# Kernel tuning notes

Measured on AMD Instinct MI355X. Metric: run time of the kernel, lower is better.

Reference implementation:

```python
import jax, jax.numpy as jnp
import numpy as np
from jax import lax

D, N, M_HIST, H, H_STU, T = 256, 128, 512, 32, 20, 256
ETA = 1e-3


def _hankel(m):
    # standard spectral-filtering Hankel: Z[i,j] = 2 / ((i+j)^3 - (i+j)), 1-indexed
    idx = np.arange(1, m + 1, dtype=np.float64)
    s = idx[:, None] + idx[None, :]
    return 2.0 / (s ** 3 - s)


def setup_inputs() -> dict:
    key = jax.random.key(0)
    ks = jax.random.split(key, 10)
    ev, evec = np.linalg.eigh(_hankel(M_HIST))
    phi = jnp.asarray(evec[:, -H:], jnp.float32)          # (m, h)
    sigma = jnp.asarray(ev[-H:], jnp.float32)             # (h,) positive
    phi_stu = jnp.asarray(evec[:, -H_STU:], jnp.float32)  # (m, 20)
    A = 0.05 * jax.random.normal(ks[0], (D, D), jnp.float32)
    B = 0.05 * jax.random.normal(ks[1], (D, N), jnp.float32)
    q = jax.random.normal(ks[2], (D, D), jnp.float32)
    Q = 0.1 * (q @ q.T) / D                                # PSD state cost
    r = jax.random.normal(ks[3], (N, N), jnp.float32)
    R = 0.1 * (r @ r.T) / N                                # PSD control cost
    K = 0.01 * jax.random.normal(ks[4], (N, D), jnp.float32)  # stand-in LQR gain
    M0 = 0.005 * jax.random.normal(ks[5], (H, N, D), jnp.float32)
    M_stu = 0.003 * jax.random.normal(ks[6], (H_STU, D, N), jnp.float32)
    x0 = 0.1 * jax.random.normal(ks[7], (D, 1), jnp.float32)
    W0 = jnp.zeros((D, M_HIST), jnp.float32).at[:, 0].set(
        0.1 * jax.random.normal(ks[8], (D,), jnp.float32))
    U0 = jnp.zeros((N, M_HIST), jnp.float32)
    return {"A": A, "B": B, "Q": Q, "R": R, "K": K, "phi": phi,
            "sigma": sigma, "phi_stu": phi_stu, "M0": M0, "M_stu": M_stu,
            "x0": x0, "W0": W0, "U0": U0}


def reference(A, B, Q, R, K, phi, sigma, phi_stu, M0, M_stu, x0, W0, U0):
    sig4 = sigma ** 0.25  # (h,)

    def step(carry, _):
        x, W, U, M = carry  # x:(d,1) W:(d,m) U:(n,m) M:(h,n,d)

        def cost_fn(M_):
            v = W @ phi                                        # (d, h)
            cn = jnp.einsum('h,hnd,dh->n', sig4, M_, v)[:, None]  # (n,1)
            u = -K @ x + cn                                    # flag=False branch
            cost = (x.T @ Q @ x + u.T @ R @ u)[0, 0]
            return cost, u

        (cost, u), gM = jax.value_and_grad(cost_fn, has_aux=True)(M)
        # u_t_history.roll + write detached u
        U2 = jnp.roll(U, 1, axis=1).at[:, 0].set(lax.stop_gradient(u)[:, 0])
        # x_next = sum_i M_stu[i] @ (U2 @ phi_stu[:, i])
        x_next = jnp.einsum('kdn,nk->d', M_stu, U2 @ phi_stu)[:, None]
        new_w = x_next - A @ x - B @ u
        W2 = jnp.roll(W, 1, axis=1).at[:, 0].set(lax.stop_gradient(new_w)[:, 0])
        M2 = M - ETA * gM  # inline SGD on M only (matches manual update)
        return (lax.stop_gradient(x_next), W2, U2, M2), cost

    _, losses = lax.scan(step, (x0, W0, U0, M0), None, length=T)
    return losses  # (T,)
```

## Files before the change

kernel.cpp:

```cpp
#include <hip/hip_runtime.h>

#define Dd 256
#define Nn 128
#define Hh 32
#define HSk 20
#define Tt 256
#define NWG 128
#define NT 256
#define ETAf 1e-3f

__device__ __forceinline__ unsigned ld_ag(const unsigned* p) {
  return __hip_atomic_load(p, __ATOMIC_RELAXED, __HIP_MEMORY_SCOPE_AGENT);
}
__device__ __forceinline__ void st_ag(unsigned* p, unsigned v) {
  __hip_atomic_store(p, v, __ATOMIC_RELAXED, __HIP_MEMORY_SCOPE_AGENT);
}
__device__ __forceinline__ float ldg_c(const float* p) {
  return __hip_atomic_load(p, __ATOMIC_RELAXED, __HIP_MEMORY_SCOPE_AGENT);
}
__device__ __forceinline__ void stg_c(float* p, float v) {
  __hip_atomic_store(p, v, __ATOMIC_RELAXED, __HIP_MEMORY_SCOPE_AGENT);
}

__device__ __forceinline__ void grid_sync(unsigned* flags, unsigned* gen, unsigned b) {
  asm volatile("s_waitcnt vmcnt(0)" ::: "memory");
  __syncthreads();
  if (blockIdx.x == 0) {
    const int t = threadIdx.x;
    if (t > 0 && t < NWG) {
      while (ld_ag(&flags[t * 16]) < b) __builtin_amdgcn_s_sleep(1);
    }
    __syncthreads();
    if (t == 0) st_ag(gen, b);
  } else if (threadIdx.x == 0) {
    st_ag(&flags[blockIdx.x * 16], b);
    while (ld_ag(gen) < b) __builtin_amdgcn_s_sleep(1);
  }
  asm volatile("" ::: "memory");
  __syncthreads();
}

__global__ void init_bar_kernel(unsigned* bar, int n) {
  for (int i = threadIdx.x; i < n; i += blockDim.x) bar[i] = 0u;
}

__global__ __launch_bounds__(NT, 1)
void osf_main(const float* __restrict__ Am, const float* __restrict__ Bm,
              const float* __restrict__ Qmat, const float* __restrict__ Rm,
              const float* __restrict__ Km, const float* __restrict__ phi,
              const float* __restrict__ sigma, const float* __restrict__ phis,
              const float* __restrict__ M0, const float* __restrict__ Ms,
              const float* __restrict__ x0, const float* __restrict__ W0,
              float* __restrict__ out, unsigned* __restrict__ bar,
              float* __restrict__ fws) {
  const int g = blockIdx.x;
  const int tid = threadIdx.x;

  unsigned* flags = bar;
  unsigned* gen = bar + NWG * 16;

  float* cnp  = fws;
  float* vbuf = cnp + Hh * Nn;
  float* phT  = vbuf + Hh * Dd;
  float* kx   = phT + HSk * Nn;
  float* xs   = kx + Nn;
  float* u2   = xs + Tt * Dd;

  __shared__ float s_u[Nn], s_part[2][Nn], s_urow[Tt], s_w[2][Tt];
  __shared__ float s_x[Dd], s_S[2][Nn], s_A[2][Dd], s_B[2][Nn], s_K[Dd];
  __shared__ float s_g[32], s_xh[2], s_red[NT], s_red4[NT], s_w0[2];

  const int h = g >> 2;
  const int n0 = (g & 3) * 32;
  const int jj = tid >> 3;
  const int dsub = tid & 7;
  const float sig4h = sqrtf(sqrtf(sigma[h]));

  for (int i = tid; i < Dd; i += NT) {
    s_A[0][i] = Am[(2 * g) * Dd + i];
    s_A[1][i] = Am[(2 * g + 1) * Dd + i];
    s_K[i] = Km[g * Dd + i];
  }
  for (int i = tid; i < Nn; i += NT) {
    float a0 = 0.f, a1 = 0.f;
    for (int k = 0; k < HSk; ++k) {
      a0 += phis[k] * Ms[(k * Dd + 2 * g) * Nn + i];
      a1 += phis[k] * Ms[(k * Dd + 2 * g + 1) * Nn + i];
    }
    s_S[0][i] = a0;
    s_S[1][i] = a1;
    s_B[0][i] = Bm[(2 * g) * Nn + i];
    s_B[1][i] = Bm[(2 * g + 1) * Nn + i];
  }
  if (tid < 2) s_w0[tid] = W0[(2 * g + tid) * 512];

  float Mreg[32], vp[32];
  {
    const float* mp = M0 + ((size_t)(h * Nn + n0 + jj) * Dd + dsub * 32);
#pragma unroll
    for (int e = 0; e < 32; ++e) {
      Mreg[e] = mp[e];
      vp[e] = 0.f;
    }
  }
  __syncthreads();

  unsigned b = 0;
  for (int t = 0;; ++t) {
    if (t > 0) {
      {
        const int n = tid & 127, hh = tid >> 7;
        float p = 0.f;
        const float* cp = cnp + (hh * 16) * Nn + n;
#pragma unroll
        for (int q = 0; q < 16; ++q) p += ldg_c(cp + q * Nn);
        s_part[hh][n] = p;
      }
      __syncthreads();
      if (tid < Nn) s_u[tid] = s_part[0][tid] + s_part[1][tid] - ldg_c(&kx[tid]);
      __syncthreads();
      if (tid < Nn && ((t - 1) & 127) == g) u2[(size_t)(t - 1) * Nn + tid] = s_u[tid];
      if (tid == 0) s_urow[t - 1] = s_u[g];
      {
        float p = 0.f;
        const float* rr = Rm + (n0 + jj) * Nn + dsub * 16;
#pragma unroll
        for (int q = 0; q < 16; ++q) p += rr[q] * s_u[dsub * 16 + q];
        p += __shfl_xor(p, 1);
        p += __shfl_xor(p, 2);
        p += __shfl_xor(p, 4);
        if (dsub == 0) s_g[jj] = 2.f * p;
      }
      if (t < Tt && tid < 128) {
        const int dd = tid >> 6, l = tid & 63;
        float pS = s_S[dd][l] * s_u[l] + s_S[dd][l + 64] * s_u[l + 64];
        float pB = s_B[dd][l] * s_u[l] + s_B[dd][l + 64] * s_u[l + 64];
        float pA = 0.f;
#pragma unroll
        for (int q = 0; q < 4; ++q) pA += s_A[dd][l + 64 * q] * s_x[l + 64 * q];
#pragma unroll
        for (int off = 1; off < 64; off <<= 1) {
          pS += __shfl_xor(pS, off);
          pB += __shfl_xor(pB, off);
          pA += __shfl_xor(pA, off);
        }
        if (l == 0) {
          const float xt = s_xh[dd] + pS;
          s_w[dd][t - 1] = xt - pA - pB;
          stg_c(&xs[(size_t)t * Dd + 2 * g + dd], xt);
        }
      }
      __syncthreads();
    }
    if (t == Tt) break;

    {
      const int ssub = tid >> 5, lane = tid & 31;
      float a4 = 0.f;
      if (t > 0 && lane < HSk) {
        for (int s = ssub; s < t; s += 8)
          a4 += s_urow[s] * phis[(t - s) * HSk + lane];
      }
      s_red4[tid] = a4;
      const int dd = tid >> 7, r = tid & 127;
      const int s5 = r >> 5, h5 = r & 31;
      float a5 = 0.f;
      for (int s = s5; s < t; s += 4)
        a5 += s_w[dd][s] * phi[(t - 1 - s) * Hh + h5];
      s_red[tid] = a5;
    }
    __syncthreads();
    if (t > 0 && tid < HSk) {
      float p = 0.f;
#pragma unroll
      for (int q = 0; q < 8; ++q) p += s_red4[q * 32 + tid];
      stg_c(&phT[tid * Nn + g], p);
    }
    if (tid < 64) {
      const int dd = tid >> 5, h5 = tid & 31;
      float v = s_w0[dd] * phi[t * Hh + h5];
#pragma unroll
      for (int q = 0; q < 4; ++q) v += s_red[dd * 128 + q * 32 + h5];
      stg_c(&vbuf[h5 * Dd + 2 * g + dd], v);
    }

    grid_sync(flags, gen, ++b);

    s_x[tid] = (t == 0) ? x0[tid] : ldg_c(&xs[(size_t)t * Dd + tid]);
    __syncthreads();

    {
      float vc[32];
      const float* vrow = vbuf + h * Dd + dsub * 32;
#pragma unroll
      for (int e = 0; e < 32; ++e) vc[e] = ldg_c(vrow + e);
      float coef = 0.f;
      if (t > 0) coef = ETAf * sig4h * s_g[jj];
      float acc = 0.f;
#pragma unroll
      for (int e = 0; e < 32; ++e) {
        Mreg[e] -= coef * vp[e];
        acc += Mreg[e] * vc[e];
        vp[e] = vc[e];
      }
      acc += __shfl_xor(acc, 1);
      acc += __shfl_xor(acc, 2);
      acc += __shfl_xor(acc, 4);
      if (dsub == 0) stg_c(&cnp[h * Nn + n0 + jj], sig4h * acc);
    }
    {
      float accx = 0.f;
      if (t > 0) {
        const int dd = tid >> 7, n = tid & 127;
        const int d = 2 * g + dd;
#pragma unroll
        for (int k = 0; k < HSk; ++k)
          accx += Ms[(k * Dd + d) * Nn + n] * ldg_c(&phT[k * Nn + n]);
      }
      float acck = s_K[tid] * s_x[tid];
#pragma unroll
      for (int off = 1; off < 64; off <<= 1) {
        accx += __shfl_xor(accx, off);
        acck += __shfl_xor(acck, off);
      }
      __syncthreads();
      if ((tid & 63) == 0) {
        s_red[tid >> 6] = accx;
        s_red[8 + (tid >> 6)] = acck;
      }
      __syncthreads();
      if (tid < 2) s_xh[tid] = s_red[2 * tid] + s_red[2 * tid + 1];
      if (tid == 0) stg_c(&kx[g], s_red[8] + s_red[9] + s_red[10] + s_red[11]);
    }

    grid_sync(flags, gen, ++b);
  }

  for (int tt = g; tt < Tt; tt += NWG) {
    __syncthreads();
    s_x[tid] = (tt == 0) ? x0[tid] : ldg_c(&xs[(size_t)tt * Dd + tid]);
    __syncthreads();
    float qp = 0.f;
    for (int d2 = 0; d2 < Dd; ++d2) qp += Qmat[d2 * Dd + tid] * s_x[d2];
    float tot = qp * s_x[tid];
    if (tid < Nn) {
      const float un = u2[(size_t)tt * Nn + tid];
      float rp = 0.f;
      for (int n2 = 0; n2 < Nn; ++n2) rp += Rm[n2 * Nn + tid] * u2[(size_t)tt * Nn + n2];
      tot += un * rp;
    }
#pragma unroll
    for (int off = 1; off < 64; off <<= 1) tot += __shfl_xor(tot, off);
    __syncthreads();
    if ((tid & 63) == 0) s_red[tid >> 6] = tot;
    __syncthreads();
    if (tid == 0) out[tt] = s_red[0] + s_red[1] + s_red[2] + s_red[3];
  }
}

extern "C" void kernel_launch(void* const* d_in, const int* in_sizes, int n_in,
                              void* d_out, int out_size, void* d_ws, size_t ws_size,
                              hipStream_t stream) {
  (void)in_sizes; (void)n_in; (void)out_size; (void)ws_size;
  const float* A   = (const float*)d_in[0];
  const float* B   = (const float*)d_in[1];
  const float* Qm  = (const float*)d_in[2];
  const float* R   = (const float*)d_in[3];
  const float* K   = (const float*)d_in[4];
  const float* phi = (const float*)d_in[5];
  const float* sig = (const float*)d_in[6];
  const float* phs = (const float*)d_in[7];
  const float* M0  = (const float*)d_in[8];
  const float* Ms  = (const float*)d_in[9];
  const float* x0  = (const float*)d_in[10];
  const float* W0  = (const float*)d_in[11];

  unsigned* bar = (unsigned*)d_ws;
  float* fws = (float*)((char*)d_ws + 12288);

  init_bar_kernel<<<1, 256, 0, stream>>>(bar, NWG * 16 + 16);
  osf_main<<<NWG, NT, 0, stream>>>(A, B, Qm, R, K, phi, sig, phs, M0, Ms, x0, W0,
                                   (float*)d_out, bar, fws);
}
```

Before: 4.371 ms.

## Replace centralized grid barrier with all-to-all flags and atomic u accumulation

The two-level master/worker grid barrier is replaced by a flat one: each block writes its own flag and polls all flags without sleeping. The per-block partial sums for u (cnp and kx) are now accumulated with float atomics into a double-buffered global vector, which removes a reduction pass and a block sync. The O(t) history convolutions for v and phT are precomputed one step ahead, after the barrier, so that only a small correction is left before the next barrier. In exchange, float atomics make the summation order nondeterministic, and busy polling raises memory traffic.

After: 5.657 ms. 29.4% more time.

```diff
diff --git a/kernel.cpp b/kernel.cpp
--- a/kernel.cpp
+++ b/kernel.cpp
@@ -21,27 +21,24 @@
 __device__ __forceinline__ void stg_c(float* p, float v) {
   __hip_atomic_store(p, v, __ATOMIC_RELAXED, __HIP_MEMORY_SCOPE_AGENT);
 }
-
-__device__ __forceinline__ void grid_sync(unsigned* flags, unsigned* gen, unsigned b) {
+__device__ __forceinline__ void atadd_c(float* p, float v) {
+  __hip_atomic_fetch_add(p, v, __ATOMIC_RELAXED, __HIP_MEMORY_SCOPE_AGENT);
+}
+
+__device__ __forceinline__ void grid_sync(unsigned* flags, unsigned b) {
   asm volatile("s_waitcnt vmcnt(0)" ::: "memory");
   __syncthreads();
-  if (blockIdx.x == 0) {
-    const int t = threadIdx.x;
-    if (t > 0 && t < NWG) {
-      while (ld_ag(&flags[t * 16]) < b) __builtin_amdgcn_s_sleep(1);
-    }
-    __syncthreads();
-    if (t == 0) st_ag(gen, b);
-  } else if (threadIdx.x == 0) {
-    st_ag(&flags[blockIdx.x * 16], b);
-    while (ld_ag(gen) < b) __builtin_amdgcn_s_sleep(1);
+  if (threadIdx.x == 0) st_ag(&flags[blockIdx.x], b);
+  if (threadIdx.x < NWG) {
+    while (ld_ag(&flags[threadIdx.x]) < b) {}
   }
   asm volatile("" ::: "memory");
   __syncthreads();
 }
 
-__global__ void init_bar_kernel(unsigned* bar, int n) {
-  for (int i = threadIdx.x; i < n; i += blockDim.x) bar[i] = 0u;
+__global__ void init_ws_kernel(unsigned* bar, float* uacc) {
+  for (int i = threadIdx.x; i < NWG; i += 256) bar[i] = 0u;
+  for (int i = threadIdx.x; i < 2 * Nn; i += 256) uacc[i] = 0.f;
 }
 
 __global__ __launch_bounds__(NT, 1)
@@ -55,20 +52,17 @@
               float* __restrict__ fws) {
   const int g = blockIdx.x;
   const int tid = threadIdx.x;
-
   unsigned* flags = bar;
-  unsigned* gen = bar + NWG * 16;
-
-  float* cnp  = fws;
-  float* vbuf = cnp + Hh * Nn;
+
+  float* uacc = fws;
+  float* vbuf = uacc + 2 * Nn;
   float* phT  = vbuf + Hh * Dd;
-  float* kx   = phT + HSk * Nn;
-  float* xs   = kx + Nn;
-  float* u2   = xs + Tt * Dd;
-
-  __shared__ float s_u[Nn], s_part[2][Nn], s_urow[Tt], s_w[2][Tt];
+  float* xs   = phT + HSk * Nn;
+  float* u2   = xs + (size_t)Tt * Dd;
+
+  __shared__ float s_u[Nn], s_urow[Tt], s_w[2][Tt];
   __shared__ float s_x[Dd], s_S[2][Nn], s_A[2][Dd], s_B[2][Nn], s_K[Dd];
-  __shared__ float s_g[32], s_xh[2], s_red[NT], s_red4[NT], s_w0[2];
+  __shared__ float s_g[32], s_xh[2], s_red[16], s_pre5[NT], s_pre4[NT], s_w0[2];
 
   const int h = g >> 2;
   const int n0 = (g & 3) * 32;
@@ -93,6 +87,8 @@
     s_B[1][i] = Bm[(2 * g + 1) * Nn + i];
   }
   if (tid < 2) s_w0[tid] = W0[(2 * g + tid) * 512];
+  s_pre5[tid] = 0.f;
+  s_pre4[tid] = 0.f;
 
   float Mreg[32], vp[32];
   {
@@ -108,16 +104,11 @@
   unsigned b = 0;
   for (int t = 0;; ++t) {
     if (t > 0) {
-      {
-        const int n = tid & 127, hh = tid >> 7;
-        float p = 0.f;
-        const float* cp = cnp + (hh * 16) * Nn + n;
-#pragma unroll
-        for (int q = 0; q < 16; ++q) p += ldg_c(cp + q * Nn);
-        s_part[hh][n] = p;
-      }
-      __syncthreads();
-      if (tid < Nn) s_u[tid] = s_part[0][tid] + s_part[1][tid] - ldg_c(&kx[tid]);
+      if (tid < Nn) {
+        const float uv = ldg_c(&uacc[(t & 1) * Nn + tid]);
+        stg_c(&uacc[(t & 1) * Nn + tid], 0.f);
+        s_u[tid] = uv;
+      }
       __syncthreads();
       if (tid < Nn && ((t - 1) & 127) == g) u2[(size_t)(t - 1) * Nn + tid] = s_u[tid];
       if (tid == 0) s_urow[t - 1] = s_u[g];
@@ -154,48 +145,57 @@
     }
     if (t == Tt) break;
 
-    {
-      const int ssub = tid >> 5, lane = tid & 31;
-      float a4 = 0.f;
-      if (t > 0 && lane < HSk) {
-        for (int s = ssub; s < t; s += 8)
-          a4 += s_urow[s] * phis[(t - s) * HSk + lane];
-      }
-      s_red4[tid] = a4;
+    if (tid < 64) {
+      const int dd = tid >> 5, h5 = tid & 31;
+      float v = s_w0[dd] * phi[t * Hh + h5];
+      if (t > 0) v += s_w[dd][t - 1] * phi[h5];
+#pragma unroll
+      for (int q = 0; q < 4; ++q) v += s_pre5[dd * 128 + q * 32 + h5];
+      stg_c(&vbuf[h5 * Dd + 2 * g + dd], v);
+    }
+    if (t > 0 && tid < HSk) {
+      float p = s_u[g] * phis[HSk + tid];
+#pragma unroll
+      for (int q = 0; q < 8; ++q) p += s_pre4[q * 32 + tid];
+      stg_c(&phT[tid * Nn + g], p);
+    }
+
+    grid_sync(flags, ++b);
+
+    const float xreg = (t == 0) ? x0[tid] : ldg_c(&xs[(size_t)t * Dd + tid]);
+
+    float vc[32];
+    {
+      const float* vrow = vbuf + h * Dd + dsub * 32;
+#pragma unroll
+      for (int e = 0; e < 32; ++e) vc[e] = ldg_c(vrow + e);
+    }
+
+    float accx = 0.f;
+    if (t > 0) {
+      const int dd = tid >> 7, n = tid & 127;
+      const int d = 2 * g + dd;
+#pragma unroll
+      for (int k = 0; k < HSk; ++k)
+        accx += Ms[((size_t)k * Dd + d) * Nn + n] * ldg_c(&phT[k * Nn + n]);
+    }
+
+    {
       const int dd = tid >> 7, r = tid & 127;
       const int s5 = r >> 5, h5 = r & 31;
       float a5 = 0.f;
-      for (int s = s5; s < t; s += 4)
-        a5 += s_w[dd][s] * phi[(t - 1 - s) * Hh + h5];
-      s_red[tid] = a5;
-    }
-    __syncthreads();
-    if (t > 0 && tid < HSk) {
-      float p = 0.f;
-#pragma unroll
-      for (int q = 0; q < 8; ++q) p += s_red4[q * 32 + tid];
-      stg_c(&phT[tid * Nn + g], p);
-    }
-    if (tid < 64) {
-      const int dd = tid >> 5, h5 = tid & 31;
-      float v = s_w0[dd] * phi[t * Hh + h5];
-#pragma unroll
-      for (int q = 0; q < 4; ++q) v += s_red[dd * 128 + q * 32 + h5];
-      stg_c(&vbuf[h5 * Dd + 2 * g + dd], v);
-    }
-
-    grid_sync(flags, gen, ++b);
-
-    s_x[tid] = (t == 0) ? x0[tid] : ldg_c(&xs[(size_t)t * Dd + tid]);
-    __syncthreads();
-
-    {
-      float vc[32];
-      const float* vrow = vbuf + h * Dd + dsub * 32;
-#pragma unroll
-      for (int e = 0; e < 32; ++e) vc[e] = ldg_c(vrow + e);
-      float coef = 0.f;
-      if (t > 0) coef = ETAf * sig4h * s_g[jj];
+      for (int s = s5; s < t; s += 4) a5 += s_w[dd][s] * phi[(t - s) * Hh + h5];
+      s_pre5[tid] = a5;
+      const int ssub = tid >> 5, lane = tid & 31;
+      float a4 = 0.f;
+      if (lane < HSk) {
+        for (int s = ssub; s < t; s += 8) a4 += s_urow[s] * phis[(t + 1 - s) * HSk + lane];
+      }
+      s_pre4[tid] = a4;
+    }
+
+    {
+      float coef = (t > 0) ? (ETAf * sig4h * s_g[jj]) : 0.f;
       float acc = 0.f;
 #pragma unroll
       for (int e = 0; e < 32; ++e) {
@@ -206,34 +206,29 @@
       acc += __shfl_xor(acc, 1);
       acc += __shfl_xor(acc, 2);
       acc += __shfl_xor(acc, 4);
-      if (dsub == 0) stg_c(&cnp[h * Nn + n0 + jj], sig4h * acc);
-    }
-    {
-      float accx = 0.f;
-      if (t > 0) {
-        const int dd = tid >> 7, n = tid & 127;
-        const int d = 2 * g + dd;
-#pragma unroll
-        for (int k = 0; k < HSk; ++k)
-          accx += Ms[(k * Dd + d) * Nn + n] * ldg_c(&phT[k * Nn + n]);
-      }
-      float acck = s_K[tid] * s_x[tid];
+      if (dsub == 0) atadd_c(&uacc[((t + 1) & 1) * Nn + n0 + jj], sig4h * acc);
+    }
+
+    {
+      float acck = s_K[tid] * xreg;
 #pragma unroll
       for (int off = 1; off < 64; off <<= 1) {
         accx += __shfl_xor(accx, off);
         acck += __shfl_xor(acck, off);
       }
-      __syncthreads();
       if ((tid & 63) == 0) {
         s_red[tid >> 6] = accx;
         s_red[8 + (tid >> 6)] = acck;
       }
+      s_x[tid] = xreg;
       __syncthreads();
       if (tid < 2) s_xh[tid] = s_red[2 * tid] + s_red[2 * tid + 1];
-      if (tid == 0) stg_c(&kx[g], s_red[8] + s_red[9] + s_red[10] + s_red[11]);
-    }
-
-    grid_sync(flags, gen, ++b);
+      if (tid == 0)
+        atadd_c(&uacc[((t + 1) & 1) * Nn + g],
+                -(s_red[8] + s_red[9] + s_red[10] + s_red[11]));
+    }
+
+    grid_sync(flags, ++b);
   }
 
   for (int tt = g; tt < Tt; tt += NWG) {
@@ -278,7 +273,7 @@
   unsigned* bar = (unsigned*)d_ws;
   float* fws = (float*)((char*)d_ws + 12288);
 
-  init_bar_kernel<<<1, 256, 0, stream>>>(bar, NWG * 16 + 16);
+  init_ws_kernel<<<1, 256, 0, stream>>>(bar, fws);
   osf_main<<<NWG, NT, 0, stream>>>(A, B, Qm, R, K, phi, sig, phs, M0, Ms, x0, W0,
                                    (float*)d_out, bar, fws);
 }
```

## Restructure persistent kernel to 32 large workgroups with all-to-all flag barriers

Applied to the files above, without the earlier changes.

Reduces the persistent grid from 128 workgroups of 256 threads to 32 workgroups of 1024 threads. The master/worker grid barrier is replaced by per-block flags that every block polls directly. Each block now owns 8 state rows and 4 control entries, and computes its control outputs locally instead of reducing partial sums through global memory. Shared v and phi-projection buffers are staged into LDS once per step. The aim is fewer and cheaper cross-workgroup synchronisations and less global traffic per step, at the cost of fewer active CUs and heavier per-block work.

Result: slower. 5.501 ms (+25.8%).

```diff
diff --git a/kernel.cpp b/kernel.cpp
--- a/kernel.cpp
+++ b/kernel.cpp
@@ -5,8 +5,8 @@
 #define Hh 32
 #define HSk 20
 #define Tt 256
-#define NWG 128
-#define NT 256
+#define NWG 32
+#define NT 1024
 #define ETAf 1e-3f
 
 __device__ __forceinline__ unsigned ld_ag(const unsigned* p) {
@@ -22,29 +22,17 @@
   __hip_atomic_store(p, v, __ATOMIC_RELAXED, __HIP_MEMORY_SCOPE_AGENT);
 }
 
-__device__ __forceinline__ void grid_sync(unsigned* flags, unsigned* gen, unsigned b) {
-  asm volatile("s_waitcnt vmcnt(0)" ::: "memory");
-  __syncthreads();
-  if (blockIdx.x == 0) {
-    const int t = threadIdx.x;
-    if (t > 0 && t < NWG) {
-      while (ld_ag(&flags[t * 16]) < b) __builtin_amdgcn_s_sleep(1);
-    }
-    __syncthreads();
-    if (t == 0) st_ag(gen, b);
-  } else if (threadIdx.x == 0) {
-    st_ag(&flags[blockIdx.x * 16], b);
-    while (ld_ag(gen) < b) __builtin_amdgcn_s_sleep(1);
-  }
-  asm volatile("" ::: "memory");
-  __syncthreads();
-}
-
-__global__ void init_bar_kernel(unsigned* bar, int n) {
-  for (int i = threadIdx.x; i < n; i += blockDim.x) bar[i] = 0u;
-}
-
-__global__ __launch_bounds__(NT, 1)
+__device__ __forceinline__ float wred64(float p) {
+  p += __shfl_xor(p, 1);  p += __shfl_xor(p, 2);  p += __shfl_xor(p, 4);
+  p += __shfl_xor(p, 8);  p += __shfl_xor(p, 16); p += __shfl_xor(p, 32);
+  return p;
+}
+
+__global__ void init_ws_kernel(unsigned* bar) {
+  for (int i = threadIdx.x; i < 2 * NWG * 16; i += 256) bar[i] = 0u;
+}
+
+__global__ __launch_bounds__(NT, 4)
 void osf_main(const float* __restrict__ Am, const float* __restrict__ Bm,
               const float* __restrict__ Qmat, const float* __restrict__ Rm,
               const float* __restrict__ Km, const float* __restrict__ phi,
@@ -56,205 +44,222 @@
   const int g = blockIdx.x;
   const int tid = threadIdx.x;
 
-  unsigned* flags = bar;
-  unsigned* gen = bar + NWG * 16;
-
-  float* cnp  = fws;
-  float* vbuf = cnp + Hh * Nn;
-  float* phT  = vbuf + Hh * Dd;
-  float* kx   = phT + HSk * Nn;
-  float* xs   = kx + Nn;
-  float* u2   = xs + Tt * Dd;
-
-  __shared__ float s_u[Nn], s_part[2][Nn], s_urow[Tt], s_w[2][Tt];
-  __shared__ float s_x[Dd], s_S[2][Nn], s_A[2][Dd], s_B[2][Nn], s_K[Dd];
-  __shared__ float s_g[32], s_xh[2], s_red[NT], s_red4[NT], s_w0[2];
-
-  const int h = g >> 2;
-  const int n0 = (g & 3) * 32;
-  const int jj = tid >> 3;
-  const int dsub = tid & 7;
+  unsigned* hflag = bar;
+  unsigned* bflag = bar + NWG * 16;
+
+  float* vpub  = fws;
+  float* phpub = vpub + Hh * Dd;
+  float* us    = phpub + HSk * Nn;
+  float* xs    = us + Tt * Nn;
+
+  const int d0 = 8 * g;
+  const int n0 = 4 * g;
+
+  const int h  = tid >> 5;
+  const int nn = (tid >> 3) & 3;
+  const int q  = tid & 7;
+
+  __shared__ float s_v[Hh * 264];
+  __shared__ float s_php[HSk * Nn];
+  __shared__ float whist[8][Tt];
+  __shared__ float uh[4][Tt];
+  __shared__ float s_S0[8][Nn];
+  __shared__ float s_u[Nn], s_x[Dd];
+  __shared__ float s_prev[8][Hh];
+  __shared__ float s_g[4], s_cn[Hh * 4], s_kx[4], s_xc8[8], s_Bu8[8], s_w8[8],
+      s_Axp[8], s_prex[8], s_red[16], s_w0v[8];
+
   const float sig4h = sqrtf(sqrtf(sigma[h]));
 
-  for (int i = tid; i < Dd; i += NT) {
-    s_A[0][i] = Am[(2 * g) * Dd + i];
-    s_A[1][i] = Am[(2 * g + 1) * Dd + i];
-    s_K[i] = Km[g * Dd + i];
-  }
-  for (int i = tid; i < Nn; i += NT) {
-    float a0 = 0.f, a1 = 0.f;
-    for (int k = 0; k < HSk; ++k) {
-      a0 += phis[k] * Ms[(k * Dd + 2 * g) * Nn + i];
-      a1 += phis[k] * Ms[(k * Dd + 2 * g + 1) * Nn + i];
-    }
-    s_S[0][i] = a0;
-    s_S[1][i] = a1;
-    s_B[0][i] = Bm[(2 * g) * Nn + i];
-    s_B[1][i] = Bm[(2 * g + 1) * Nn + i];
-  }
-  if (tid < 2) s_w0[tid] = W0[(2 * g + tid) * 512];
+  {
+    const int dp = tid >> 7, j = tid & 127;
+    float a = 0.f;
+    for (int k = 0; k < HSk; ++k)
+      a += phis[k] * Ms[((size_t)k * Dd + d0 + dp) * Nn + j];
+    s_S0[dp][j] = a;
+    if (tid < 256) {
+      const int dp2 = tid >> 5, hh = tid & 31;
+      s_prev[dp2][hh] = W0[(d0 + dp2) * 512] * phi[hh];
+    }
+    if (tid < 8) {
+      s_w0v[tid] = W0[(d0 + tid) * 512];
+      s_w8[tid] = 0.f; s_prex[tid] = 0.f; s_Axp[tid] = 0.f;
+    }
+  }
 
   float Mreg[32], vp[32];
   {
-    const float* mp = M0 + ((size_t)(h * Nn + n0 + jj) * Dd + dsub * 32);
-#pragma unroll
-    for (int e = 0; e < 32; ++e) {
-      Mreg[e] = mp[e];
-      vp[e] = 0.f;
-    }
+    const float* mp = M0 + ((size_t)(h * Nn + n0 + nn) * Dd + q * 32);
+#pragma unroll
+    for (int e = 0; e < 32; ++e) { Mreg[e] = mp[e]; vp[e] = 0.f; }
   }
   __syncthreads();
 
-  unsigned b = 0;
-  for (int t = 0;; ++t) {
+  for (int t = 0; t < Tt; ++t) {
     if (t > 0) {
-      {
-        const int n = tid & 127, hh = tid >> 7;
+      if (tid < Nn) s_u[tid] = ldg_c(&us[(t - 1) * Nn + tid]);
+      __syncthreads();
+      if (tid < 4) uh[tid][t - 1] = s_u[n0 + tid];
+      if (tid < 256) {
+        const int np = tid >> 6, c = tid & 63;
+        float p = Rm[(n0 + np) * Nn + c] * s_u[c] +
+                  Rm[(n0 + np) * Nn + c + 64] * s_u[c + 64];
+        p = wred64(p);
+        if ((tid & 63) == 0) s_g[np] = 2.f * p;
+      } else if (tid < 512) {
+        const int r = tid - 256, dp = r >> 5, l = r & 31;
         float p = 0.f;
-        const float* cp = cnp + (hh * 16) * Nn + n;
-#pragma unroll
-        for (int q = 0; q < 16; ++q) p += ldg_c(cp + q * Nn);
-        s_part[hh][n] = p;
-      }
-      __syncthreads();
-      if (tid < Nn) s_u[tid] = s_part[0][tid] + s_part[1][tid] - ldg_c(&kx[tid]);
-      __syncthreads();
-      if (tid < Nn && ((t - 1) & 127) == g) u2[(size_t)(t - 1) * Nn + tid] = s_u[tid];
-      if (tid == 0) s_urow[t - 1] = s_u[g];
-      {
+        for (int j2 = 0; j2 < 4; ++j2) p += s_S0[dp][l + 32 * j2] * s_u[l + 32 * j2];
+        p += __shfl_xor(p, 1); p += __shfl_xor(p, 2); p += __shfl_xor(p, 4);
+        p += __shfl_xor(p, 8); p += __shfl_xor(p, 16);
+        if (l == 0) s_xc8[dp] = s_prex[dp] + p;
+      } else if (tid < 768) {
+        const int r = tid - 512, dp = r >> 5, l = r & 31;
         float p = 0.f;
-        const float* rr = Rm + (n0 + jj) * Nn + dsub * 16;
-#pragma unroll
-        for (int q = 0; q < 16; ++q) p += rr[q] * s_u[dsub * 16 + q];
-        p += __shfl_xor(p, 1);
-        p += __shfl_xor(p, 2);
-        p += __shfl_xor(p, 4);
-        if (dsub == 0) s_g[jj] = 2.f * p;
-      }
-      if (t < Tt && tid < 128) {
-        const int dd = tid >> 6, l = tid & 63;
-        float pS = s_S[dd][l] * s_u[l] + s_S[dd][l + 64] * s_u[l + 64];
-        float pB = s_B[dd][l] * s_u[l] + s_B[dd][l + 64] * s_u[l + 64];
-        float pA = 0.f;
-#pragma unroll
-        for (int q = 0; q < 4; ++q) pA += s_A[dd][l + 64 * q] * s_x[l + 64 * q];
-#pragma unroll
-        for (int off = 1; off < 64; off <<= 1) {
-          pS += __shfl_xor(pS, off);
-          pB += __shfl_xor(pB, off);
-          pA += __shfl_xor(pA, off);
-        }
-        if (l == 0) {
-          const float xt = s_xh[dd] + pS;
-          s_w[dd][t - 1] = xt - pA - pB;
-          stg_c(&xs[(size_t)t * Dd + 2 * g + dd], xt);
-        }
-      }
-      __syncthreads();
-    }
-    if (t == Tt) break;
+        for (int j2 = 0; j2 < 4; ++j2)
+          p += Bm[(d0 + dp) * Nn + l + 32 * j2] * s_u[l + 32 * j2];
+        p += __shfl_xor(p, 1); p += __shfl_xor(p, 2); p += __shfl_xor(p, 4);
+        p += __shfl_xor(p, 8); p += __shfl_xor(p, 16);
+        if (l == 0) s_Bu8[dp] = p;
+      }
+      __syncthreads();
+      if (tid < 8) {
+        const float wv = s_xc8[tid] - s_Axp[tid] - s_Bu8[tid];
+        whist[tid][t - 1] = wv;
+        s_w8[tid] = wv;
+      }
+      __syncthreads();
+    }
+
+    if (tid < 256) {
+      const int dp = tid >> 5, hh = tid & 31;
+      stg_c(&vpub[hh * Dd + d0 + dp], s_prev[dp][hh] + s_w8[dp] * phi[hh]);
+    } else if (tid < 264) {
+      if (t > 0) stg_c(&xs[(size_t)t * Dd + d0 + (tid - 256)], s_xc8[tid - 256]);
+    } else if (tid >= 320 && tid < 960) {
+      const int r = tid - 320;
+      const int np = r / 160, rem = r - np * 160, k = rem >> 3, sub = rem & 7;
+      float p = 0.f;
+      for (int s = sub; s < t; s += 8) p += uh[np][s] * phis[(t - s) * HSk + k];
+      p += __shfl_xor(p, 1); p += __shfl_xor(p, 2); p += __shfl_xor(p, 4);
+      if (sub == 0) stg_c(&phpub[k * Nn + n0 + np], p);
+    }
+    asm volatile("s_waitcnt vmcnt(0)" ::: "memory");
+    __syncthreads();
+    if (tid == 0) st_ag(&hflag[g * 16], (unsigned)(t + 1));
+
+    if (tid < NWG) {
+      while (ld_ag(&hflag[tid * 16]) < (unsigned)(t + 1)) __builtin_amdgcn_s_sleep(1);
+    }
+    asm volatile("" ::: "memory");
+    __syncthreads();
+#pragma unroll
+    for (int i = 0; i < 8; ++i) {
+      const int idx = tid * 8 + i;
+      const int hh = idx >> 8, dl = idx & 255;
+      s_v[hh * 264 + dl + (dl >> 5)] = ldg_c(&vpub[idx]);
+    }
+    if (tid < 256) s_x[tid] = (t == 0) ? x0[tid] : ldg_c(&xs[(size_t)t * Dd + tid]);
+    if (tid < 640) {
+#pragma unroll
+      for (int i = 0; i < 4; ++i) {
+        const int idx = tid * 4 + i;
+        s_php[idx] = ldg_c(&phpub[idx]);
+      }
+    }
+    __syncthreads();
 
     {
-      const int ssub = tid >> 5, lane = tid & 31;
-      float a4 = 0.f;
-      if (t > 0 && lane < HSk) {
-        for (int s = ssub; s < t; s += 8)
-          a4 += s_urow[s] * phis[(t - s) * HSk + lane];
-      }
-      s_red4[tid] = a4;
-      const int dd = tid >> 7, r = tid & 127;
-      const int s5 = r >> 5, h5 = r & 31;
-      float a5 = 0.f;
-      for (int s = s5; s < t; s += 4)
-        a5 += s_w[dd][s] * phi[(t - 1 - s) * Hh + h5];
-      s_red[tid] = a5;
-    }
-    __syncthreads();
-    if (t > 0 && tid < HSk) {
+      const float coef = (t > 0) ? (ETAf * sig4h * s_g[nn]) : 0.f;
+      float acc = 0.f;
+      const float* vrow = &s_v[h * 264 + q * 33];
+#pragma unroll
+      for (int e = 0; e < 32; ++e) {
+        const float vce = vrow[e];
+        Mreg[e] -= coef * vp[e];
+        acc += Mreg[e] * vce;
+        vp[e] = vce;
+      }
+      acc += __shfl_xor(acc, 1); acc += __shfl_xor(acc, 2); acc += __shfl_xor(acc, 4);
+      if (q == 0) s_cn[h * 4 + nn] = sig4h * acc;
+    }
+    if (tid < 256) {
+      const int np = tid >> 6, c = tid & 63;
       float p = 0.f;
-#pragma unroll
-      for (int q = 0; q < 8; ++q) p += s_red4[q * 32 + tid];
-      stg_c(&phT[tid * Nn + g], p);
-    }
-    if (tid < 64) {
-      const int dd = tid >> 5, h5 = tid & 31;
-      float v = s_w0[dd] * phi[t * Hh + h5];
-#pragma unroll
-      for (int q = 0; q < 4; ++q) v += s_red[dd * 128 + q * 32 + h5];
-      stg_c(&vbuf[h5 * Dd + 2 * g + dd], v);
-    }
-
-    grid_sync(flags, gen, ++b);
-
-    s_x[tid] = (t == 0) ? x0[tid] : ldg_c(&xs[(size_t)t * Dd + tid]);
-    __syncthreads();
+      for (int j2 = 0; j2 < 4; ++j2)
+        p += Km[(n0 + np) * Dd + c + 64 * j2] * s_x[c + 64 * j2];
+      p = wred64(p);
+      if ((tid & 63) == 0) s_kx[np] = p;
+    }
+    __syncthreads();
+    if (tid < 4) {
+      float uu = -s_kx[tid];
+      for (int hh = 0; hh < Hh; ++hh) uu += s_cn[hh * 4 + tid];
+      stg_c(&us[(size_t)t * Nn + n0 + tid], uu);
+    }
+    asm volatile("s_waitcnt vmcnt(0)" ::: "memory");
+    __syncthreads();
+    if (tid == 0) st_ag(&bflag[g * 16], (unsigned)(t + 1));
 
     {
-      float vc[32];
-      const float* vrow = vbuf + h * Dd + dsub * 32;
-#pragma unroll
-      for (int e = 0; e < 32; ++e) vc[e] = ldg_c(vrow + e);
-      float coef = 0.f;
-      if (t > 0) coef = ETAf * sig4h * s_g[jj];
-      float acc = 0.f;
-#pragma unroll
-      for (int e = 0; e < 32; ++e) {
-        Mreg[e] -= coef * vp[e];
-        acc += Mreg[e] * vc[e];
-        vp[e] = vc[e];
-      }
-      acc += __shfl_xor(acc, 1);
-      acc += __shfl_xor(acc, 2);
-      acc += __shfl_xor(acc, 4);
-      if (dsub == 0) stg_c(&cnp[h * Nn + n0 + jj], sig4h * acc);
-    }
-    {
-      float accx = 0.f;
-      if (t > 0) {
-        const int dd = tid >> 7, n = tid & 127;
-        const int d = 2 * g + dd;
-#pragma unroll
-        for (int k = 0; k < HSk; ++k)
-          accx += Ms[(k * Dd + d) * Nn + n] * ldg_c(&phT[k * Nn + n]);
-      }
-      float acck = s_K[tid] * s_x[tid];
-#pragma unroll
-      for (int off = 1; off < 64; off <<= 1) {
-        accx += __shfl_xor(accx, off);
-        acck += __shfl_xor(acck, off);
-      }
-      __syncthreads();
-      if ((tid & 63) == 0) {
-        s_red[tid >> 6] = accx;
-        s_red[8 + (tid >> 6)] = acck;
-      }
-      __syncthreads();
-      if (tid < 2) s_xh[tid] = s_red[2 * tid] + s_red[2 * tid + 1];
-      if (tid == 0) stg_c(&kx[g], s_red[8] + s_red[9] + s_red[10] + s_red[11]);
-    }
-
-    grid_sync(flags, gen, ++b);
+      const int dp = tid >> 7;
+      const int r = tid & 127, hh = r >> 2, sub = r & 3;
+      float p = 0.f;
+      for (int s = sub; s < t; s += 4)
+        p += whist[dp][s] * phi[(t - s) * Hh + hh];
+      p += __shfl_xor(p, 1); p += __shfl_xor(p, 2);
+
+      const int j = tid & 127;
+      float fx = 0.f;
+      for (int k = 0; k < HSk; ++k)
+        fx += Ms[((size_t)k * Dd + d0 + dp) * Nn + j] * s_php[k * Nn + j];
+      fx = wred64(fx);
+
+      float ax = 0.f;
+      if (tid < 512) {
+        const int dp2 = tid >> 6, c = tid & 63;
+        for (int j2 = 0; j2 < 4; ++j2)
+          ax += Am[(d0 + dp2) * Dd + c + 64 * j2] * s_x[c + 64 * j2];
+        ax = wred64(ax);
+      }
+      if (sub == 0) s_prev[dp][hh] = p + s_w0v[dp] * phi[(t + 1) * Hh + hh];
+      if ((tid & 63) == 0) s_red[tid >> 6] = fx;
+      if (tid < 512 && (tid & 63) == 0) s_Axp[tid >> 6] = ax;
+      __syncthreads();
+      if (tid < 8) s_prex[tid] = s_red[2 * tid] + s_red[2 * tid + 1];
+    }
+
+    if (tid < NWG) {
+      while (ld_ag(&bflag[tid * 16]) < (unsigned)(t + 1)) __builtin_amdgcn_s_sleep(1);
+    }
+    asm volatile("" ::: "memory");
+    __syncthreads();
   }
 
   for (int tt = g; tt < Tt; tt += NWG) {
     __syncthreads();
-    s_x[tid] = (tt == 0) ? x0[tid] : ldg_c(&xs[(size_t)tt * Dd + tid]);
-    __syncthreads();
-    float qp = 0.f;
-    for (int d2 = 0; d2 < Dd; ++d2) qp += Qmat[d2 * Dd + tid] * s_x[d2];
-    float tot = qp * s_x[tid];
-    if (tid < Nn) {
-      const float un = u2[(size_t)tt * Nn + tid];
+    if (tid < 256) s_x[tid] = (tt == 0) ? x0[tid] : ldg_c(&xs[(size_t)tt * Dd + tid]);
+    if (tid < 128) s_u[tid] = ldg_c(&us[(size_t)tt * Nn + tid]);
+    __syncthreads();
+    float tot = 0.f;
+    if (tid < 256) {
+      float qp = 0.f;
+      for (int d2 = 0; d2 < Dd; ++d2) qp += Qmat[d2 * Dd + tid] * s_x[d2];
+      tot = qp * s_x[tid];
+    }
+    if (tid < 128) {
       float rp = 0.f;
-      for (int n2 = 0; n2 < Nn; ++n2) rp += Rm[n2 * Nn + tid] * u2[(size_t)tt * Nn + n2];
-      tot += un * rp;
-    }
-#pragma unroll
-    for (int off = 1; off < 64; off <<= 1) tot += __shfl_xor(tot, off);
-    __syncthreads();
+      for (int n2 = 0; n2 < Nn; ++n2) rp += Rm[n2 * Nn + tid] * s_u[n2];
+      tot += s_u[tid] * rp;
+    }
+    tot = wred64(tot);
     if ((tid & 63) == 0) s_red[tid >> 6] = tot;
     __syncthreads();
-    if (tid == 0) out[tt] = s_red[0] + s_red[1] + s_red[2] + s_red[3];
+    if (tid == 0) {
+      float ss = 0.f;
+      for (int i2 = 0; i2 < 16; ++i2) ss += s_red[i2];
+      out[tt] = ss;
+    }
   }
 }
 
@@ -276,9 +281,9 @@
   const float* W0  = (const float*)d_in[11];
 
   unsigned* bar = (unsigned*)d_ws;
-  float* fws = (float*)((char*)d_ws + 12288);
-
-  init_bar_kernel<<<1, 256, 0, stream>>>(bar, NWG * 16 + 16);
+  float* fws = (float*)((char*)d_ws + 4096);
+
+  init_ws_kernel<<<1, 256, 0, stream>>>(bar);
   osf_main<<<NWG, NT, 0, stream>>>(A, B, Qm, R, K, phi, sig, phs, M0, Ms, x0, W0,
                                    (float*)d_out, bar, fws);
 }
```
